# Kernel optimization log

Hardware: AMD Instinct MI355X
Metric: run time of the kernel (lower is better)

Reference implementation:

```python
import jax, jax.numpy as jnp
import numpy as np

D_MODEL = 128; D_STATE = 64; D_CONV = 4; EXPAND = 2; HEADDIM = 32; NGROUPS = 1
D_INNER = EXPAND * D_MODEL            # 256
NHEADS = D_INNER // HEADDIM           # 8
CONV_DIM = D_INNER + 2 * NGROUPS * D_STATE   # 384 (x, B, C streams)
D_IN_PROJ = 2 * D_INNER + 2 * NGROUPS * D_STATE + NHEADS  # 648 (z, xBC, dt)
EPS = 1e-5


def setup_inputs() -> dict:
    key = jax.random.key(0)
    ks = jax.random.split(key, 8)
    B, L = 8, 4096
    x = jax.random.normal(ks[0], (B, L, D_MODEL), jnp.float32)
    norm_w = jnp.ones((D_MODEL,), jnp.float32)
    in_proj_w = jax.random.normal(ks[1], (D_IN_PROJ, D_MODEL), jnp.float32) * (D_MODEL ** -0.5)
    conv_w = jax.random.normal(ks[2], (CONV_DIM, D_CONV), jnp.float32) * (D_CONV ** -0.5)
    conv_b = jnp.zeros((CONV_DIM,), jnp.float32)
    dt_bias = jax.random.uniform(ks[3], (NHEADS,), jnp.float32, -4.0, -1.0)
    A_log = jnp.log(jax.random.uniform(ks[4], (NHEADS,), jnp.float32, 1.0, 16.0))
    D = jnp.ones((NHEADS,), jnp.float32)
    gnorm_w = jnp.ones((D_INNER,), jnp.float32)
    out_proj_w = jax.random.normal(ks[5], (D_MODEL, D_INNER), jnp.float32) * (D_INNER ** -0.5)
    return dict(x=x, norm_w=norm_w, in_proj_w=in_proj_w, conv_w=conv_w, conv_b=conv_b,
                dt_bias=dt_bias, A_log=A_log, D=D, gnorm_w=gnorm_w, out_proj_w=out_proj_w)


def _rmsnorm(x, w):
    return x * jax.lax.rsqrt(jnp.mean(x * x, axis=-1, keepdims=True) + EPS) * w


def _causal_dw_conv(x, w, b):
    # x: [B,L,C]; w: [C,K]; depthwise causal conv along L
    K = w.shape[1]
    xp = jnp.pad(x, ((0, 0), (K - 1, 0), (0, 0)))
    kern = jnp.transpose(w)[:, None, :]  # [K,1,C] for WIO with groups=C
    out = jax.lax.conv_general_dilated(
        xp, kern, window_strides=(1,), padding='VALID',
        dimension_numbers=('NWC', 'WIO', 'NWC'),
        feature_group_count=w.shape[0])
    return out + b


def _ssm(xh, dt, Bm, Cm, A):
    # xh: [B,L,H,P]; dt: [B,L,H]; Bm, Cm: [B,L,N]; A: [H]
    def step(h, inp):
        x_t, dt_t, B_t, C_t = inp
        dA = jnp.exp(dt_t * A)                                   # [B,H]
        h = h * dA[..., None, None] + (dt_t[..., None] * x_t)[..., None] * B_t[:, None, None, :]
        y = jnp.einsum('bhpn,bn->bhp', h, C_t)
        return h, y
    Bsz, L, H, P = xh.shape
    N = Bm.shape[-1]
    h0 = jnp.zeros((Bsz, H, P, N), xh.dtype)
    xs = (xh.transpose(1, 0, 2, 3), dt.transpose(1, 0, 2),
          Bm.transpose(1, 0, 2), Cm.transpose(1, 0, 2))
    _, ys = jax.lax.scan(step, h0, xs)
    return ys.transpose(1, 0, 2, 3)  # [B,L,H,P]


def reference(x, norm_w, in_proj_w, conv_w, conv_b, dt_bias, A_log, D, gnorm_w, out_proj_w):
    xn = _rmsnorm(x, norm_w)
    zxbcdt = xn @ in_proj_w.T                                    # [B,L,648]
    z, xBC, dt = jnp.split(zxbcdt, [D_INNER, D_INNER + CONV_DIM], axis=-1)
    dt = jax.nn.softplus(dt + dt_bias)                           # [B,L,H]
    xBC = jax.nn.silu(_causal_dw_conv(xBC, conv_w, conv_b))
    xs, Bm, Cm = jnp.split(xBC, [D_INNER, D_INNER + NGROUPS * D_STATE], axis=-1)
    Bsz, L, _ = x.shape
    xh = xs.reshape(Bsz, L, NHEADS, HEADDIM)
    A = -jnp.exp(A_log)                                          # [H]
    y = _ssm(xh, dt, Bm, Cm, A) + D[None, None, :, None] * xh    # D skip per head
    y = y.reshape(Bsz, L, D_INNER)
    y = _rmsnorm(y * jax.nn.silu(z), gnorm_w)                    # gated RMSNorm
    out = y @ out_proj_w.T
    return x + out
```

## Files before the change

### kernel.cpp

```cpp
#include <hip/hip_runtime.h>

#define DM    128
#define DI    256
#define NH    8
#define HD    32
#define NS    64
#define CDIM  384
#define DPROJ 648
#define LSEQ  4096
#define NB    8
#define NTOK  32768
#define LC    64
#define NC    64
#define EPSF  1e-5f
#define LOG2E 1.4426950408889634f

typedef __bf16 bf16;
typedef bf16  bf16x8 __attribute__((ext_vector_type(8)));
typedef bf16  bf16x4 __attribute__((ext_vector_type(4)));
typedef short short8 __attribute__((ext_vector_type(8)));
typedef float f32x4  __attribute__((ext_vector_type(4)));

__device__ __forceinline__ unsigned short f2bfbits(float f) {
    unsigned int u = __float_as_uint(f);
    unsigned int r = u + 0x7FFFu + ((u >> 16) & 1u);
    return (unsigned short)(r >> 16);
}
__device__ __forceinline__ float bfbits2f(unsigned short u) {
    return __uint_as_float(((unsigned int)u) << 16);
}

__global__ __launch_bounds__(256) void k_cast(const float* __restrict__ in,
                                              unsigned short* __restrict__ out, int n) {
    int i = blockIdx.x * 256 + threadIdx.x;
    if (i < n) out[i] = f2bfbits(in[i]);
}

__global__ __launch_bounds__(256) void k_rmsdt(const float* __restrict__ x,
                                               const float* __restrict__ w,
                                               const float* __restrict__ w1,
                                               const float* __restrict__ dtb,
                                               unsigned short* __restrict__ xnb,
                                               float* __restrict__ dtf) {
    __shared__ float Xs[4][132];
    __shared__ float Wd[8][132];
    const int t = threadIdx.x;
    {
        int row = t >> 5, col = (t & 31) * 4;
        *(float4*)&Wd[row][col] = *(const float4*)(w1 + (size_t)(640 + row) * DM + col);
    }
    const int wave = t >> 6, lane = t & 63;
    const size_t row = (size_t)blockIdx.x * 4 + wave;
    const float* xr = x + row * DM + lane * 2;
    float v0 = xr[0], v1 = xr[1];
    float ss = v0 * v0 + v1 * v1;
    #pragma unroll
    for (int o = 32; o; o >>= 1) ss += __shfl_xor(ss, o);
    float r = rsqrtf(ss * (1.0f / DM) + EPSF);
    float o0 = v0 * r * w[lane * 2], o1 = v1 * r * w[lane * 2 + 1];
    Xs[wave][lane * 2] = o0; Xs[wave][lane * 2 + 1] = o1;
    ushort2 ob; ob.x = f2bfbits(o0); ob.y = f2bfbits(o1);
    *(ushort2*)(xnb + row * DM + lane * 2) = ob;
    __syncthreads();
    const int h = lane >> 3, ks = lane & 7;
    float acc = 0.f;
    #pragma unroll
    for (int i = 0; i < 4; i++) {
        float4 xv = *(const float4*)&Xs[wave][ks * 16 + i * 4];
        float4 wv = *(const float4*)&Wd[h][ks * 16 + i * 4];
        acc = fmaf(xv.x, wv.x, acc);
        acc = fmaf(xv.y, wv.y, acc);
        acc = fmaf(xv.z, wv.z, acc);
        acc = fmaf(xv.w, wv.w, acc);
    }
    acc += __shfl_xor(acc, 1);
    acc += __shfl_xor(acc, 2);
    acc += __shfl_xor(acc, 4);
    if (ks == 0) {
        float v = acc + dtb[h];
        dtf[row * NH + h] = (v > 20.f) ? v : log1pf(expf(v));
    }
}

__global__ __launch_bounds__(256) void k_gemm1(const unsigned short* __restrict__ A,
                                               const unsigned short* __restrict__ B,
                                               unsigned short* __restrict__ zb,
                                               unsigned short* __restrict__ xbc) {
    __shared__ bf16 As[64 * 40];
    __shared__ bf16 Bs[64 * 40];
    const int t = threadIdx.x;
    const int m0 = blockIdx.x * 64, n0 = blockIdx.y * 64;
    const int wave = t >> 6, lane = t & 63;
    const int wm = wave >> 1, wn = wave & 1;
    const int fr = lane & 15, fk = (lane >> 4) * 8;
    f32x4 acc[2][2] = {};
    const int r = t >> 2, q = (t & 3) * 8;
    for (int k0 = 0; k0 < DM; k0 += 32) {
        __syncthreads();
        *(short8*)&As[r * 40 + q] = *(const short8*)(A + (size_t)(m0 + r) * DM + k0 + q);
        short8 bv = {};
        if (n0 + r < DPROJ) bv = *(const short8*)(B + (size_t)(n0 + r) * DM + k0 + q);
        *(short8*)&Bs[r * 40 + q] = bv;
        __syncthreads();
        #pragma unroll
        for (int mt = 0; mt < 2; mt++) {
            bf16x8 af = *(const bf16x8*)&As[(wm * 32 + mt * 16 + fr) * 40 + fk];
            #pragma unroll
            for (int nt = 0; nt < 2; nt++) {
                bf16x8 bf = *(const bf16x8*)&Bs[(wn * 32 + nt * 16 + fr) * 40 + fk];
                acc[mt][nt] = __builtin_amdgcn_mfma_f32_16x16x32_bf16(af, bf, acc[mt][nt], 0, 0, 0);
            }
        }
    }
    #pragma unroll
    for (int mt = 0; mt < 2; mt++)
        #pragma unroll
        for (int nt = 0; nt < 2; nt++) {
            int n = n0 + wn * 32 + nt * 16 + fr;
            if (n >= 640) continue;
            #pragma unroll
            for (int rr = 0; rr < 4; rr++) {
                int m = m0 + wm * 32 + mt * 16 + (lane >> 4) * 4 + rr;
                unsigned short v = f2bfbits(acc[mt][nt][rr]);
                if (n < DI) zb[(size_t)m * DI + n] = v;
                else        xbc[(size_t)m * CDIM + (n - 256)] = v;
            }
        }
}

__global__ __launch_bounds__(384) void k_conv(const unsigned short* __restrict__ xbc,
                                              const float* __restrict__ cw,
                                              const float* __restrict__ cb,
                                              unsigned short* __restrict__ xcb) {
    const int c = threadIdx.x;
    const int t0 = blockIdx.x * 64;
    const int l0 = t0 & (LSEQ - 1);
    float4 wv = *(const float4*)(cw + c * 4);
    float bias = cb[c];
    const unsigned short* in = xbc + (size_t)t0 * CDIM + c;
    unsigned short* out = xcb + (size_t)t0 * CDIM + c;
    float h1 = 0.f, h2 = 0.f, h3 = 0.f;
    if (l0) {
        h1 = bfbits2f(in[-CDIM]);
        h2 = bfbits2f(in[-2 * CDIM]);
        h3 = bfbits2f(in[-3 * CDIM]);
    }
    #pragma unroll 4
    for (int t = 0; t < 64; t++) {
        float x0 = bfbits2f(in[(size_t)t * CDIM]);
        float acc = bias;
        acc = fmaf(x0, wv.w, acc);
        acc = fmaf(h1, wv.z, acc);
        acc = fmaf(h2, wv.y, acc);
        acc = fmaf(h3, wv.x, acc);
        float s = acc / (1.f + expf(-acc));
        out[(size_t)t * CDIM] = f2bfbits(s);
        h3 = h2; h2 = h1; h1 = x0;
    }
}

__global__ __launch_bounds__(256, 2) void k_ssd1(const unsigned short* __restrict__ xcb,
                                                 const float* __restrict__ dtf,
                                                 const float* __restrict__ alog,
                                                 unsigned short* __restrict__ hst,
                                                 float* __restrict__ dAp) {
    __shared__ bf16 Wl[4][64 * 72];
    __shared__ bf16 Xl[4][64 * 40];
    __shared__ float wl[4][64];
    const int bh = blockIdx.x >> 4, cg = blockIdx.x & 15;
    const int b = bh >> 3, h = bh & 7;
    const int wave = threadIdx.x >> 6, lane = threadIdx.x & 63;
    const int c = cg * 4 + wave;
    const size_t tok0 = (size_t)b * LSEQ + c * LC;
    const float A = -expf(alog[h]);
    float dt = dtf[(tok0 + lane) * NH + h];
    float q = dt * A * LOG2E;
    #pragma unroll
    for (int o = 1; o <= 32; o <<= 1) {
        float tmp = __shfl_up(q, o);
        if (lane >= o) q += tmp;
    }
    float qL = __shfl(q, 63);
    wl[wave][lane] = exp2f(qL - q) * dt;
    const unsigned short* xrow = xcb + tok0 * CDIM;
    #pragma unroll
    for (int it = 0; it < 4; it++) {
        int f = it * 64 + lane, r = f >> 2, c8 = (f & 3) * 8;
        *(bf16x8*)&Xl[wave][r * 40 + c8] = *(const bf16x8*)(xrow + (size_t)r * CDIM + h * HD + c8);
    }
    #pragma unroll
    for (int it = 0; it < 8; it++) {
        int f = it * 64 + lane, r = f >> 3, c8 = (f & 7) * 8;
        float w = wl[wave][r];
        bf16x8 v = *(const bf16x8*)(xrow + (size_t)r * CDIM + 256 + c8);
        bf16x8 o;
        #pragma unroll
        for (int j = 0; j < 8; j++) o[j] = (bf16)((float)v[j] * w);
        *(bf16x8*)&Wl[wave][r * 72 + c8] = o;
    }
    const int m = lane & 15, ko = lane >> 4;
    f32x4 hacc[4][2] = {};
    #pragma unroll
    for (int kh = 0; kh < 2; kh++) {
        bf16x8 xb[2];
        #pragma unroll
        for (int pi = 0; pi < 2; pi++)
            #pragma unroll
            for (int j = 0; j < 8; j++)
                xb[pi][j] = Xl[wave][(kh * 32 + ko * 8 + j) * 40 + pi * 16 + m];
        #pragma unroll
        for (int ni = 0; ni < 4; ni++) {
            bf16x8 af;
            #pragma unroll
            for (int j = 0; j < 8; j++)
                af[j] = Wl[wave][(kh * 32 + ko * 8 + j) * 72 + ni * 16 + m];
            #pragma unroll
            for (int pi = 0; pi < 2; pi++)
                hacc[ni][pi] = __builtin_amdgcn_mfma_f32_16x16x32_bf16(af, xb[pi], hacc[ni][pi], 0, 0, 0);
        }
    }
    unsigned short* hb = hst + (((size_t)bh * NC + c) << 11);
    #pragma unroll
    for (int ni = 0; ni < 4; ni++)
        #pragma unroll
        for (int pi = 0; pi < 2; pi++)
            #pragma unroll
            for (int r = 0; r < 4; r++)
                hb[(ni * 16 + ko * 4 + r) * 32 + pi * 16 + m] = f2bfbits(hacc[ni][pi][r]);
    if (lane == 0) dAp[(size_t)bh * NC + c] = exp2f(qL);
}

__global__ __launch_bounds__(256) void k_ssm2(unsigned short* __restrict__ hst,
                                              const float* __restrict__ dAp) {
    __shared__ float dl[2][NC];
    const int pr = blockIdx.x >> 3, seg = blockIdx.x & 7;
    const int bh0 = pr * 2, bh1 = pr * 2 + 1;
    const int s = seg * 256 + threadIdx.x;
    if (threadIdx.x < NC) dl[0][threadIdx.x] = dAp[(size_t)bh0 * NC + threadIdx.x];
    else if (threadIdx.x < 2 * NC) dl[1][threadIdx.x - NC] = dAp[(size_t)bh1 * NC + threadIdx.x - NC];
    __syncthreads();
    unsigned short* b0 = hst + ((size_t)bh0 * NC << 11) + s;
    unsigned short* b1 = hst + ((size_t)bh1 * NC << 11) + s;
    float r0 = 0.f, r1 = 0.f;
    float n0 = bfbits2f(b0[0]), n1 = bfbits2f(b1[0]);
    for (int c = 0; c < NC; c++) {
        float t0 = n0, t1 = n1;
        if (c + 1 < NC) {
            n0 = bfbits2f(b0[(size_t)(c + 1) << 11]);
            n1 = bfbits2f(b1[(size_t)(c + 1) << 11]);
        }
        b0[(size_t)c << 11] = f2bfbits(r0);
        b1[(size_t)c << 11] = f2bfbits(r1);
        r0 = fmaf(r0, dl[0][c], t0);
        r1 = fmaf(r1, dl[1][c], t1);
    }
}

__global__ __launch_bounds__(256, 2) void k_ssd3(const unsigned short* __restrict__ xcb,
                                                 const float* __restrict__ dtf,
                                                 const float* __restrict__ alog,
                                                 const unsigned short* __restrict__ hst,
                                                 const float* __restrict__ Dw,
                                                 unsigned short* __restrict__ ybb) {
    __shared__ bf16 Pl[4][64 * 72];
    __shared__ bf16 Xl[4][64 * 40];
    __shared__ bf16 Hl[4][64 * 40];
    __shared__ float ql[4][64];
    __shared__ float dl[4][64];
    const int bh = blockIdx.x >> 4, cg = blockIdx.x & 15;
    const int b = bh >> 3, h = bh & 7;
    const int wave = threadIdx.x >> 6, lane = threadIdx.x & 63;
    const int c = cg * 4 + wave;
    const size_t tok0 = (size_t)b * LSEQ + c * LC;
    const float A = -expf(alog[h]);
    const float Dh = Dw[h];
    float dt = dtf[(tok0 + lane) * NH + h];
    float q = dt * A * LOG2E;
    #pragma unroll
    for (int o = 1; o <= 32; o <<= 1) {
        float tmp = __shfl_up(q, o);
        if (lane >= o) q += tmp;
    }
    ql[wave][lane] = q;
    dl[wave][lane] = dt;
    const unsigned short* xrow = xcb + tok0 * CDIM;
    #pragma unroll
    for (int it = 0; it < 4; it++) {
        int f = it * 64 + lane, r = f >> 2, c8 = (f & 3) * 8;
        *(bf16x8*)&Xl[wave][r * 40 + c8] = *(const bf16x8*)(xrow + (size_t)r * CDIM + h * HD + c8);
    }
    const unsigned short* hbg = hst + (((size_t)bh * NC + c) << 11);
    #pragma unroll
    for (int it = 0; it < 4; it++) {
        int f = it * 64 + lane, n = f >> 2, p8 = (f & 3) * 8;
        *(bf16x8*)&Hl[wave][n * 40 + p8] = *(const bf16x8*)(hbg + f * 8);
    }
    const int m = lane & 15, ko = lane >> 4;
    bf16x8 cf[4][2];
    #pragma unroll
    for (int ti = 0; ti < 4; ti++)
        #pragma unroll
        for (int kh = 0; kh < 2; kh++)
            cf[ti][kh] = *(const bf16x8*)(xrow + (size_t)(ti * 16 + m) * CDIM + 320 + kh * 32 + ko * 8);
    f32x4 g[4][4] = {};
    #pragma unroll
    for (int kh = 0; kh < 2; kh++) {
        bf16x8 bfg[4];
        #pragma unroll
        for (int si = 0; si < 4; si++)
            bfg[si] = *(const bf16x8*)(xrow + (size_t)(si * 16 + m) * CDIM + 256 + kh * 32 + ko * 8);
        #pragma unroll
        for (int ti = 0; ti < 4; ti++)
            #pragma unroll
            for (int si = 0; si < 4; si++)
                g[ti][si] = __builtin_amdgcn_mfma_f32_16x16x32_bf16(cf[ti][kh], bfg[si], g[ti][si], 0, 0, 0);
    }
    __syncthreads();
    float qt[4][4], et[4][4];
    #pragma unroll
    for (int ti = 0; ti < 4; ti++)
        #pragma unroll
        for (int r = 0; r < 4; r++) {
            float v = ql[wave][ti * 16 + ko * 4 + r];
            qt[ti][r] = v; et[ti][r] = exp2f(v);
        }
    float qs[4], ds[4];
    #pragma unroll
    for (int si = 0; si < 4; si++) {
        qs[si] = ql[wave][si * 16 + m];
        ds[si] = dl[wave][si * 16 + m];
    }
    #pragma unroll
    for (int ti = 0; ti < 4; ti++)
        #pragma unroll
        for (int si = 0; si < 4; si++)
            #pragma unroll
            for (int r = 0; r < 4; r++) {
                int t = ti * 16 + ko * 4 + r, s = si * 16 + m;
                float p = 0.f;
                if (si <= ti) {
                    float w = (s <= t) ? exp2f(qt[ti][r] - qs[si]) * ds[si] : 0.f;
                    p = g[ti][si][r] * w;
                    if (s == t) p += Dh;
                }
                Pl[wave][t * 72 + s] = (bf16)p;
            }
    f32x4 ya[4][2] = {}, ua[4][2] = {};
    #pragma unroll
    for (int kh = 0; kh < 2; kh++) {
        bf16x8 xb[2], hb2[2];
        #pragma unroll
        for (int pi = 0; pi < 2; pi++)
            #pragma unroll
            for (int j = 0; j < 8; j++) {
                int kk = kh * 32 + ko * 8 + j;
                xb[pi][j]  = Xl[wave][kk * 40 + pi * 16 + m];
                hb2[pi][j] = Hl[wave][kk * 40 + pi * 16 + m];
            }
        #pragma unroll
        for (int ti = 0; ti < 4; ti++) {
            bf16x8 pa = *(const bf16x8*)&Pl[wave][(ti * 16 + m) * 72 + kh * 32 + ko * 8];
            #pragma unroll
            for (int pi = 0; pi < 2; pi++) {
                ya[ti][pi] = __builtin_amdgcn_mfma_f32_16x16x32_bf16(pa, xb[pi], ya[ti][pi], 0, 0, 0);
                ua[ti][pi] = __builtin_amdgcn_mfma_f32_16x16x32_bf16(cf[ti][kh], hb2[pi], ua[ti][pi], 0, 0, 0);
            }
        }
    }
    unsigned short* yrow = ybb + tok0 * DI + h * HD;
    #pragma unroll
    for (int ti = 0; ti < 4; ti++)
        #pragma unroll
        for (int pi = 0; pi < 2; pi++)
            #pragma unroll
            for (int r = 0; r < 4; r++) {
                int t = ti * 16 + ko * 4 + r;
                yrow[(size_t)t * DI + pi * 16 + m] =
                    f2bfbits(ya[ti][pi][r] + et[ti][r] * ua[ti][pi][r]);
            }
}

__global__ __launch_bounds__(256) void k_gemm2g(const unsigned short* __restrict__ ybb,
                                                const unsigned short* __restrict__ zb,
                                                const float* __restrict__ gw,
                                                const unsigned short* __restrict__ w2b,
                                                const float* __restrict__ xin,
                                                float* __restrict__ out) {
    __shared__ bf16 As[64 * 264];
    __shared__ bf16 Bs[128 * 72];
    __shared__ float gwl[256];
    __shared__ float ssb[64][4];
    __shared__ float rsb[64];
    const int t = threadIdx.x;
    const int m0 = blockIdx.x * 64;
    gwl[t] = gw[t];
    const int r = t >> 2, q = (t & 3) * 64;
    const unsigned short* yrow = ybb + (size_t)(m0 + r) * DI + q;
    const unsigned short* zrow = zb + (size_t)(m0 + r) * DI + q;
    float ss = 0.f;
    #pragma unroll
    for (int i = 0; i < 8; i++) {
        bf16x8 yv = *(const bf16x8*)(yrow + i * 8);
        bf16x8 zv = *(const bf16x8*)(zrow + i * 8);
        bf16x8 g8;
        #pragma unroll
        for (int j = 0; j < 8; j++) {
            float z = (float)zv[j];
            float g = (float)yv[j] * (z / (1.f + expf(-z)));
            ss += g * g;
            g8[j] = (bf16)g;
        }
        *(bf16x8*)&As[r * 264 + q + i * 8] = g8;
    }
    ssb[r][t & 3] = ss;
    __syncthreads();
    if (t < 64) {
        float s = ssb[t][0] + ssb[t][1] + ssb[t][2] + ssb[t][3];
        rsb[t] = rsqrtf(s * (1.0f / DI) + EPSF);
    }
    __syncthreads();
    const float rs = rsb[r];
    #pragma unroll
    for (int i = 0; i < 8; i++) {
        bf16x8 g8 = *(const bf16x8*)&As[r * 264 + q + i * 8];
        #pragma unroll
        for (int j = 0; j < 8; j++)
            g8[j] = (bf16)((float)g8[j] * rs * gwl[q + i * 8 + j]);
        *(bf16x8*)&As[r * 264 + q + i * 8] = g8;
    }
    const int wave = t >> 6, lane = t & 63;
    const int wm = wave >> 1, wn = wave & 1;
    const int fr = lane & 15, fk = (lane >> 4) * 8;
    f32x4 acc[2][4] = {};
    for (int k0 = 0; k0 < DI; k0 += 64) {
        __syncthreads();
        #pragma unroll
        for (int i = 0; i < 4; i++) {
            int f = i * 256 + t, row = f >> 3, c8 = (f & 7) * 8;
            *(short8*)&Bs[row * 72 + c8] = *(const short8*)((const unsigned short*)w2b + (size_t)row * DI + k0 + c8);
        }
        __syncthreads();
        #pragma unroll
        for (int kk = 0; kk < 64; kk += 32) {
            #pragma unroll
            for (int mt = 0; mt < 2; mt++) {
                bf16x8 af = *(const bf16x8*)&As[(wm * 32 + mt * 16 + fr) * 264 + k0 + kk + fk];
                #pragma unroll
                for (int nt = 0; nt < 4; nt++) {
                    bf16x8 bf = *(const bf16x8*)&Bs[(wn * 64 + nt * 16 + fr) * 72 + kk + fk];
                    acc[mt][nt] = __builtin_amdgcn_mfma_f32_16x16x32_bf16(af, bf, acc[mt][nt], 0, 0, 0);
                }
            }
        }
    }
    #pragma unroll
    for (int mt = 0; mt < 2; mt++)
        #pragma unroll
        for (int nt = 0; nt < 4; nt++) {
            int n = wn * 64 + nt * 16 + fr;
            #pragma unroll
            for (int rr = 0; rr < 4; rr++) {
                int m = m0 + wm * 32 + mt * 16 + (lane >> 4) * 4 + rr;
                out[(size_t)m * DM + n] = xin[(size_t)m * DM + n] + acc[mt][nt][rr];
            }
        }
}

extern "C" void kernel_launch(void* const* d_in, const int* in_sizes, int n_in,
                              void* d_out, int out_size, void* d_ws, size_t ws_size,
                              hipStream_t stream) {
    const float* x   = (const float*)d_in[0];
    const float* nw  = (const float*)d_in[1];
    const float* w1  = (const float*)d_in[2];
    const float* cw  = (const float*)d_in[3];
    const float* cb  = (const float*)d_in[4];
    const float* dtb = (const float*)d_in[5];
    const float* al  = (const float*)d_in[6];
    const float* Dw  = (const float*)d_in[7];
    const float* gw  = (const float*)d_in[8];
    const float* w2  = (const float*)d_in[9];
    float* out = (float*)d_out;

    float* ws = (float*)d_ws;
    float*  dAp = ws;
    float*  dtf = dAp + NB * NH * NC;
    unsigned short* hst = (unsigned short*)(dtf + (size_t)NTOK * NH);
    unsigned short* zb  = hst + (size_t)NB * NH * NC * 2048;
    unsigned short* xbc = zb + (size_t)NTOK * DI;
    unsigned short* xcb = xbc + (size_t)NTOK * CDIM;
    unsigned short* ybb = xcb + (size_t)NTOK * CDIM;
    unsigned short* w1b = ybb + (size_t)NTOK * DI;
    unsigned short* w2b = w1b + (size_t)DPROJ * DM;
    unsigned short* xnb = ybb;

    k_cast<<<(DPROJ * DM + 255) / 256, 256, 0, stream>>>(w1, w1b, DPROJ * DM);
    k_cast<<<(DM * DI + 255) / 256, 256, 0, stream>>>(w2, w2b, DM * DI);
    k_rmsdt<<<NTOK / 4, 256, 0, stream>>>(x, nw, w1, dtb, xnb, dtf);
    k_gemm1<<<dim3(NTOK / 64, (DPROJ + 63) / 64), 256, 0, stream>>>(xnb, w1b, zb, xbc);
    k_conv<<<NTOK / 64, 384, 0, stream>>>(xbc, cw, cb, xcb);
    k_ssd1<<<NB * NH * (NC / 4), 256, 0, stream>>>(xcb, dtf, al, hst, dAp);
    k_ssm2<<<(NB * NH / 2) * 8, 256, 0, stream>>>(hst, dAp);
    k_ssd3<<<NB * NH * (NC / 4), 256, 0, stream>>>(xcb, dtf, al, hst, Dw, ybb);
    k_gemm2g<<<NTOK / 64, 256, 0, stream>>>(ybb, zb, gw, w2b, x, out);
}
```

Baseline: 195.6 us.

## Keep gated-norm activations in registers and read out_proj weights from global

The out-projection GEMM kernel is restructured so each wave owns 16 rows and keeps the gated, normalized activations in registers as MFMA A-fragments. This removes the LDS staging of both the activation tile and the weight tile. The RMS reduction now uses wave shuffles instead of shared-memory partial sums. Weight fragments are loaded directly from global memory (expected to hit L1/L2 since the weight is 64KB) with no inter-wave reuse, and a launch-bounds occupancy hint is added.

```diff
diff --git a/kernel.cpp b/kernel.cpp
--- a/kernel.cpp
+++ b/kernel.cpp
@@ -380,90 +380,63 @@
             }
 }
 
-__global__ __launch_bounds__(256) void k_gemm2g(const unsigned short* __restrict__ ybb,
-                                                const unsigned short* __restrict__ zb,
-                                                const float* __restrict__ gw,
-                                                const unsigned short* __restrict__ w2b,
-                                                const float* __restrict__ xin,
-                                                float* __restrict__ out) {
-    __shared__ bf16 As[64 * 264];
-    __shared__ bf16 Bs[128 * 72];
+__global__ __launch_bounds__(256, 4) void k_gemm2g(const unsigned short* __restrict__ ybb,
+                                                   const unsigned short* __restrict__ zb,
+                                                   const float* __restrict__ gw,
+                                                   const unsigned short* __restrict__ w2b,
+                                                   const float* __restrict__ xin,
+                                                   float* __restrict__ out) {
     __shared__ float gwl[256];
-    __shared__ float ssb[64][4];
-    __shared__ float rsb[64];
     const int t = threadIdx.x;
-    const int m0 = blockIdx.x * 64;
     gwl[t] = gw[t];
-    const int r = t >> 2, q = (t & 3) * 64;
-    const unsigned short* yrow = ybb + (size_t)(m0 + r) * DI + q;
-    const unsigned short* zrow = zb + (size_t)(m0 + r) * DI + q;
+    const int wave = t >> 6, lane = t & 63;
+    const int fr = lane & 15, ko = lane >> 4;
+    const int m0 = blockIdx.x * 64 + wave * 16;
+    const size_t rowo = (size_t)(m0 + fr) * DI;
     float ss = 0.f;
-    #pragma unroll
-    for (int i = 0; i < 8; i++) {
-        bf16x8 yv = *(const bf16x8*)(yrow + i * 8);
-        bf16x8 zv = *(const bf16x8*)(zrow + i * 8);
-        bf16x8 g8;
+    bf16x8 gb[8];
+    #pragma unroll
+    for (int kk = 0; kk < 8; kk++) {
+        int co = kk * 32 + ko * 8;
+        bf16x8 yv = *(const bf16x8*)(ybb + rowo + co);
+        bf16x8 zv = *(const bf16x8*)(zb + rowo + co);
         #pragma unroll
         for (int j = 0; j < 8; j++) {
             float z = (float)zv[j];
             float g = (float)yv[j] * (z / (1.f + expf(-z)));
             ss += g * g;
-            g8[j] = (bf16)g;
-        }
-        *(bf16x8*)&As[r * 264 + q + i * 8] = g8;
-    }
-    ssb[r][t & 3] = ss;
+            gb[kk][j] = (bf16)g;
+        }
+    }
+    ss += __shfl_xor(ss, 16);
+    ss += __shfl_xor(ss, 32);
+    const float rs = rsqrtf(ss * (1.0f / DI) + EPSF);
     __syncthreads();
-    if (t < 64) {
-        float s = ssb[t][0] + ssb[t][1] + ssb[t][2] + ssb[t][3];
-        rsb[t] = rsqrtf(s * (1.0f / DI) + EPSF);
-    }
-    __syncthreads();
-    const float rs = rsb[r];
-    #pragma unroll
-    for (int i = 0; i < 8; i++) {
-        bf16x8 g8 = *(const bf16x8*)&As[r * 264 + q + i * 8];
+    #pragma unroll
+    for (int kk = 0; kk < 8; kk++) {
+        int co = kk * 32 + ko * 8;
         #pragma unroll
         for (int j = 0; j < 8; j++)
-            g8[j] = (bf16)((float)g8[j] * rs * gwl[q + i * 8 + j]);
-        *(bf16x8*)&As[r * 264 + q + i * 8] = g8;
-    }
-    const int wave = t >> 6, lane = t & 63;
-    const int wm = wave >> 1, wn = wave & 1;
-    const int fr = lane & 15, fk = (lane >> 4) * 8;
-    f32x4 acc[2][4] = {};
-    for (int k0 = 0; k0 < DI; k0 += 64) {
-        __syncthreads();
-        #pragma unroll
-        for (int i = 0; i < 4; i++) {
-            int f = i * 256 + t, row = f >> 3, c8 = (f & 7) * 8;
-            *(short8*)&Bs[row * 72 + c8] = *(const short8*)((const unsigned short*)w2b + (size_t)row * DI + k0 + c8);
-        }
-        __syncthreads();
-        #pragma unroll
-        for (int kk = 0; kk < 64; kk += 32) {
-            #pragma unroll
-            for (int mt = 0; mt < 2; mt++) {
-                bf16x8 af = *(const bf16x8*)&As[(wm * 32 + mt * 16 + fr) * 264 + k0 + kk + fk];
-                #pragma unroll
-                for (int nt = 0; nt < 4; nt++) {
-                    bf16x8 bf = *(const bf16x8*)&Bs[(wn * 64 + nt * 16 + fr) * 72 + kk + fk];
-                    acc[mt][nt] = __builtin_amdgcn_mfma_f32_16x16x32_bf16(af, bf, acc[mt][nt], 0, 0, 0);
-                }
-            }
-        }
-    }
-    #pragma unroll
-    for (int mt = 0; mt < 2; mt++)
-        #pragma unroll
-        for (int nt = 0; nt < 4; nt++) {
-            int n = wn * 64 + nt * 16 + fr;
-            #pragma unroll
-            for (int rr = 0; rr < 4; rr++) {
-                int m = m0 + wm * 32 + mt * 16 + (lane >> 4) * 4 + rr;
-                out[(size_t)m * DM + n] = xin[(size_t)m * DM + n] + acc[mt][nt][rr];
-            }
-        }
+            gb[kk][j] = (bf16)((float)gb[kk][j] * rs * gwl[co + j]);
+    }
+    f32x4 acc[8] = {};
+    #pragma unroll
+    for (int kk = 0; kk < 8; kk++) {
+        #pragma unroll
+        for (int nt = 0; nt < 8; nt++) {
+            bf16x8 bfr = *(const bf16x8*)(w2b + (size_t)(nt * 16 + fr) * DI + kk * 32 + ko * 8);
+            acc[nt] = __builtin_amdgcn_mfma_f32_16x16x32_bf16(gb[kk], bfr, acc[nt], 0, 0, 0);
+        }
+    }
+    #pragma unroll
+    for (int nt = 0; nt < 8; nt++) {
+        int n = nt * 16 + fr;
+        #pragma unroll
+        for (int rr = 0; rr < 4; rr++) {
+            int m = m0 + ko * 4 + rr;
+            out[(size_t)m * DM + n] = xin[(size_t)m * DM + n] + acc[nt][rr];
+        }
+    }
 }
 
 extern "C" void kernel_launch(void* const* d_in, const int* in_sizes, int n_in,
```

Result: slower. 205.9 us (+5.3%).
